# Kernel optimization log

Measured on AMD Instinct MI355X. Metric: run time of the kernel, lower is better.

Reference implementation:

```python
import jax, jax.numpy as jnp
import numpy as np

B, S, H = 32, 2048, 1024

def setup_inputs() -> dict:
    key = jax.random.key(0)
    k0, k1, k2, k3 = jax.random.split(key, 4)
    hidden = jax.random.normal(k0, (B, H), dtype=jnp.float32)
    encoder_outputs = jax.random.normal(k1, (S, B, H), dtype=jnp.float32)
    # torch nn.Linear weight layout: [out_features, in_features]
    attn_W = jax.random.normal(k2, (H, 2 * H), dtype=jnp.float32) * (1.0 / np.sqrt(2 * H))
    attn_b = jnp.zeros((H,), dtype=jnp.float32)
    v_W = jax.random.normal(k3, (1, H), dtype=jnp.float32) * (1.0 / np.sqrt(H))
    return {"hidden": hidden, "encoder_outputs": encoder_outputs,
            "attn_W": attn_W, "attn_b": attn_b, "v_W": v_W}

def reference(hidden, encoder_outputs, attn_W, attn_b, v_W):
    # encoder_outputs: [S, B, H] -> [B, S, H]
    enc = jnp.transpose(encoder_outputs, (1, 0, 2))
    b, s, h = enc.shape
    # broadcast decoder hidden across seq dim (avoids explicit repeat copy)
    hid = jnp.broadcast_to(hidden[:, None, :], (b, s, h))
    cat = jnp.concatenate([hid, enc], axis=2)              # [B, S, 2H]
    energy = jnp.tanh(jnp.einsum('bsk,hk->bsh', cat, attn_W) + attn_b)  # [B, S, H]
    scores = jnp.einsum('bsh,oh->bso', energy, v_W)[..., 0]            # [B, S]
    attn_weights = jax.nn.softmax(scores, axis=1)                       # [B, S]
    context = jnp.einsum('bs,bsh->bh', attn_weights, enc)               # [B, H]
    return context, attn_weights
```

## Files before the change

kernel.cpp:

```cpp
#include <hip/hip_runtime.h>
#include <hip/hip_bf16.h>
#include <cstddef>

#define B_ 32
#define S_ 2048
#define H_ 1024

typedef short short8 __attribute__((ext_vector_type(8)));
typedef float floatx4 __attribute__((ext_vector_type(4)));

__device__ inline unsigned int cvt_pk_bf16(float a, float b) {
    unsigned int r;
    asm("v_cvt_pk_bf16_f32 %0, %1, %2" : "=v"(r) : "v"(a), "v"(b));
    return r;
}

__device__ inline void gload_lds16(const unsigned short* g, unsigned short* l) {
    __builtin_amdgcn_global_load_lds(
        (const __attribute__((address_space(1))) unsigned int*)g,
        (__attribute__((address_space(3))) unsigned int*)l, 16, 0, 0);
}

__global__ void prep_kernel(const float* __restrict__ enc, unsigned short* __restrict__ encT,
                            const float* __restrict__ W, unsigned short* __restrict__ Bp) {
    int bid = blockIdx.x, t = threadIdx.x;
    if (bid < 32768) {
        int gtid = bid * 256 + t;
        int m = gtid >> 7, j7 = gtid & 127;
        const float4* p = reinterpret_cast<const float4*>(enc + (size_t)m * H_ + j7 * 8);
        float4 v0 = p[0], v1 = p[1];
        union { short8 s; unsigned int u[4]; } o;
        o.u[0] = cvt_pk_bf16(v0.x, v0.y);
        o.u[1] = cvt_pk_bf16(v0.z, v0.w);
        o.u[2] = cvt_pk_bf16(v1.x, v1.y);
        o.u[3] = cvt_pk_bf16(v1.z, v1.w);
        int tile = (m >> 7) * 16 + (j7 >> 3);
        int r = m & 127;
        int j = (j7 & 7) ^ (r & 7);
        reinterpret_cast<short8*>(encT)[(size_t)tile * 1024 + r * 8 + j] = o.s;
    } else {
        int gtid = (bid - 32768) * 256 + t;
        int n = gtid >> 7, j7 = gtid & 127;
        const float4* p = reinterpret_cast<const float4*>(W + (size_t)n * 2048 + 1024 + j7 * 8);
        float4 v0 = p[0], v1 = p[1];
        union { short8 s; unsigned int u[4]; } o;
        o.u[0] = cvt_pk_bf16(v0.x, v0.y);
        o.u[1] = cvt_pk_bf16(v0.z, v0.w);
        o.u[2] = cvt_pk_bf16(v1.x, v1.y);
        o.u[3] = cvt_pk_bf16(v1.z, v1.w);
        int nb = n >> 4, lr = n & 15, kt2 = j7 >> 2, lg = j7 & 3;
        reinterpret_cast<short8*>(Bp)[(nb * 32 + kt2) * 64 + lg * 16 + lr] = o.s;
    }
}

__global__ void hid_proj_kernel(const float* __restrict__ hidden,
                                const float* __restrict__ W,
                                const float* __restrict__ bias,
                                float* __restrict__ hp) {
    int h = blockIdx.x;
    int t = threadIdx.x;
    __shared__ float red[32][257];
    __shared__ float red2[32][8];
    float psum[32];
#pragma unroll
    for (int b = 0; b < 32; b++) psum[b] = 0.f;
    const float* wrow = W + (size_t)h * 2048;
    for (int c = 0; c < 4; c++) {
        int k = c * 256 + t;
        float w = wrow[k];
#pragma unroll
        for (int b = 0; b < 32; b++) psum[b] += hidden[b * 1024 + k] * w;
    }
#pragma unroll
    for (int b = 0; b < 32; b++) red[b][t] = psum[b];
    __syncthreads();
    {
        int b = t >> 3, j = t & 7;
        float s = 0.f;
#pragma unroll
        for (int q = 0; q < 32; q++) s += red[b][j * 32 + q];
        red2[b][j] = s;
    }
    __syncthreads();
    if (t < 32) {
        float tot = 0.f;
#pragma unroll
        for (int j = 0; j < 8; j++) tot += red2[t][j];
        hp[t * 1024 + h] = tot + bias[h];
    }
}

__global__ __launch_bounds__(256, 3) void score_gemm_t(
    const unsigned short* __restrict__ encT,
    const unsigned short* __restrict__ Bp,
    const float* __restrict__ hp,
    const float* __restrict__ vw,
    float* __restrict__ scores)
{
    __shared__ alignas(16) unsigned short As[2][8192];

    const int tid = threadIdx.x;
    const int lane = tid & 63;
    const int w = tid >> 6, wr = w >> 1, wc = w & 1;
    const int lr = lane & 15, lg = lane >> 4;
    const int lx = lr & 7;

    const int bid = blockIdx.x;
    const int x = bid & 7, j = bid >> 3;
    const int nt = j & 7;
    const int mt = (j >> 3) * 8 + x;

    const unsigned short* aT = encT + (size_t)mt * 16 * 8192;
    const short8* bp8 = reinterpret_cast<const short8*>(Bp);

    short8 bpf[2][8];
    {
        const unsigned short* src = aT + (w * 4) * 512 + lane * 8;
        unsigned short* dst = &As[0][(w * 4) * 512];
#pragma unroll
        for (int i = 0; i < 4; i++) gload_lds16(src + i * 512, dst + i * 512);
#pragma unroll
        for (int kk = 0; kk < 2; kk++)
#pragma unroll
            for (int ni = 0; ni < 4; ni++) {
                int nb = nt * 8 + wc * 4 + ni;
                bpf[0][kk * 4 + ni] = bp8[(nb * 32 + kk) * 64 + lane];
            }
    }

    floatx4 acc[4][4];
#pragma unroll
    for (int mi = 0; mi < 4; mi++)
#pragma unroll
        for (int ni = 0; ni < 4; ni++) acc[mi][ni] = (floatx4)0.f;

#pragma unroll
    for (int kt = 0; kt < 16; kt++) {
        const int cb = kt & 1;
        __syncthreads();
        if (kt < 15) {
            const unsigned short* src = aT + (kt + 1) * 8192 + (w * 4) * 512 + lane * 8;
            unsigned short* dst = &As[cb ^ 1][(w * 4) * 512];
#pragma unroll
            for (int i = 0; i < 4; i++) gload_lds16(src + i * 512, dst + i * 512);
#pragma unroll
            for (int kk = 0; kk < 2; kk++)
#pragma unroll
                for (int ni = 0; ni < 4; ni++) {
                    int nb = nt * 8 + wc * 4 + ni;
                    bpf[cb ^ 1][kk * 4 + ni] = bp8[(nb * 32 + (kt + 1) * 2 + kk) * 64 + lane];
                }
        }
#pragma unroll
        for (int kk = 0; kk < 2; kk++) {
            short8 afr[4];
#pragma unroll
            for (int mi = 0; mi < 4; mi++)
                afr[mi] = *reinterpret_cast<const short8*>(
                    &As[cb][(wr * 64 + mi * 16 + lr) * 64 + ((kk * 4 + lg) ^ lx) * 8]);
#pragma unroll
            for (int mi = 0; mi < 4; mi++)
#pragma unroll
                for (int ni = 0; ni < 4; ni++)
                    acc[mi][ni] = __builtin_amdgcn_mfma_f32_16x16x32_bf16(
                        afr[mi], bpf[cb][kk * 4 + ni], acc[mi][ni], 0, 0, 0);
        }
    }

    const int colBase = nt * 128 + wc * 64;
    float vv[4];
#pragma unroll
    for (int ni = 0; ni < 4; ni++) vv[ni] = vw[colBase + ni * 16 + lr];
#pragma unroll
    for (int mi = 0; mi < 4; mi++) {
        const int rowm = wr * 64 + mi * 16 + lg * 4;
#pragma unroll
        for (int i = 0; i < 4; i++) {
            const int m = mt * 128 + rowm + i;
            const int b = m & 31, sidx = m >> 5;
            const float* hprow = hp + b * H_ + colBase;
            float s = 0.f;
#pragma unroll
            for (int ni = 0; ni < 4; ni++) {
                float e = acc[mi][ni][i] + hprow[ni * 16 + lr];
                float e2 = __expf(2.0f * e);
                float th = 1.0f - 2.0f * __builtin_amdgcn_rcpf(e2 + 1.0f);
                s += th * vv[ni];
            }
            s += __shfl_xor(s, 1, 16);
            s += __shfl_xor(s, 2, 16);
            s += __shfl_xor(s, 4, 16);
            s += __shfl_xor(s, 8, 16);
            if (lr == 0) atomicAdd(&scores[b * S_ + sidx], s);
        }
    }
}

__global__ void softmax_kernel(const float* __restrict__ scores, float* __restrict__ out) {
    int b = blockIdx.x, t = threadIdx.x;
    __shared__ float red[16];
    const float* row = scores + b * S_;
    float vals[8];
    float lmax = -1e30f;
#pragma unroll
    for (int i = 0; i < 8; i++) { vals[i] = row[i * 256 + t]; lmax = fmaxf(lmax, vals[i]); }
#pragma unroll
    for (int off = 32; off; off >>= 1) lmax = fmaxf(lmax, __shfl_xor(lmax, off, 64));
    if ((t & 63) == 0) red[t >> 6] = lmax;
    __syncthreads();
    float gmax = fmaxf(fmaxf(red[0], red[1]), fmaxf(red[2], red[3]));
    float lsum = 0.f;
#pragma unroll
    for (int i = 0; i < 8; i++) { vals[i] = __expf(vals[i] - gmax); lsum += vals[i]; }
#pragma unroll
    for (int off = 32; off; off >>= 1) lsum += __shfl_xor(lsum, off, 64);
    if ((t & 63) == 0) red[8 + (t >> 6)] = lsum;
    __syncthreads();
    float inv = 1.0f / (red[8] + red[9] + red[10] + red[11]);
#pragma unroll
    for (int i = 0; i < 8; i++) out[b * S_ + i * 256 + t] = vals[i] * inv;
}

__global__ void context_tiled(const unsigned short* __restrict__ encT,
                              const float* __restrict__ wts,
                              float* __restrict__ ctx) {
    int t = threadIdx.x;
    int hc = blockIdx.x & 1;
    int b = (blockIdx.x >> 1) & 31;
    int sc = blockIdx.x >> 6;
    int h = hc * 512 + t * 2;
    const float* w = wts + b * S_ + sc * 128;
    const int jconst = ((h >> 3) & 7) ^ (b & 7);
    const int inrow = jconst * 8 + (h & 7);
    const int ktile = h >> 6;
    float acc0 = 0.f, acc1 = 0.f;
#pragma unroll 4
    for (int s = 0; s < 128; s++) {
        int m = (sc * 128 + s) * 32 + b;
        size_t off = ((size_t)(m >> 7) * 16 + ktile) * 8192 + (m & 127) * 64 + inrow;
        unsigned int u = *reinterpret_cast<const unsigned int*>(encT + off);
        float ws_ = w[s];
        acc0 += ws_ * __uint_as_float(u << 16);
        acc1 += ws_ * __uint_as_float(u & 0xffff0000u);
    }
    atomicAdd(&ctx[b * H_ + h], acc0);
    atomicAdd(&ctx[b * H_ + h + 1], acc1);
}

__global__ void pack_w2_rm(const float* __restrict__ W, unsigned short* __restrict__ W2) {
    int i = blockIdx.x * 256 + threadIdx.x;
    int n = i >> 8;
    int k4 = (i & 255) * 4;
    float4 v = *reinterpret_cast<const float4*>(W + (size_t)n * 2048 + 1024 + k4);
    uint2 o;
    o.x = cvt_pk_bf16(v.x, v.y);
    o.y = cvt_pk_bf16(v.z, v.w);
    *reinterpret_cast<uint2*>(W2 + (size_t)n * 1024 + k4) = o;
}

__global__ __launch_bounds__(256, 3) void score_gemm_f32(
    const float* __restrict__ Ap, const unsigned short* __restrict__ W2,
    const float* __restrict__ hp, const float* __restrict__ vw,
    float* __restrict__ scores)
{
    __shared__ alignas(16) unsigned short As[128 * 64];
    __shared__ alignas(16) unsigned short Bs[128 * 64];
    const int tid = threadIdx.x;
    const int lane = tid & 63;
    const int w = tid >> 6, wr = w >> 1, wc = w & 1;
    const int lr = lane & 15, lg = lane >> 4;
    const int bid = blockIdx.x;
    const int nt = bid & 7, mt = bid >> 3;
    const int row = tid >> 1, half = tid & 1;
    const int xk = row & 7;
    const int lx = lr & 7;
    const float* aF = Ap + (size_t)(mt * 128 + row) * H_ + half * 32;
    const unsigned short* bP = W2 + (size_t)(nt * 128 + row) * H_ + half * 32;
    short8 b8[4]; float4 af[8];
    {
        const float4* p = reinterpret_cast<const float4*>(aF);
#pragma unroll
        for (int i = 0; i < 8; i++) af[i] = p[i];
        const short8* q = reinterpret_cast<const short8*>(bP);
#pragma unroll
        for (int i = 0; i < 4; i++) b8[i] = q[i];
    }
    floatx4 acc[4][4];
#pragma unroll
    for (int mi = 0; mi < 4; mi++)
#pragma unroll
        for (int ni = 0; ni < 4; ni++) acc[mi][ni] = (floatx4)0.f;
    for (int kt = 0; kt < 16; kt++) {
        __syncthreads();
#pragma unroll
        for (int i = 0; i < 4; i++) {
            union { short8 s; unsigned int u[4]; } o;
            o.u[0] = cvt_pk_bf16(af[2 * i].x, af[2 * i].y);
            o.u[1] = cvt_pk_bf16(af[2 * i].z, af[2 * i].w);
            o.u[2] = cvt_pk_bf16(af[2 * i + 1].x, af[2 * i + 1].y);
            o.u[3] = cvt_pk_bf16(af[2 * i + 1].z, af[2 * i + 1].w);
            *reinterpret_cast<short8*>(&As[row * 64 + ((half * 4 + i) ^ xk) * 8]) = o.s;
        }
#pragma unroll
        for (int i = 0; i < 4; i++)
            *reinterpret_cast<short8*>(&Bs[row * 64 + ((half * 4 + i) ^ xk) * 8]) = b8[i];
        __syncthreads();
        if (kt < 15) {
            const float4* p = reinterpret_cast<const float4*>(aF + (kt + 1) * 64);
#pragma unroll
            for (int i = 0; i < 8; i++) af[i] = p[i];
            const short8* q = reinterpret_cast<const short8*>(bP + (kt + 1) * 64);
#pragma unroll
            for (int i = 0; i < 4; i++) b8[i] = q[i];
        }
#pragma unroll
        for (int kk = 0; kk < 2; kk++) {
            const int g = (kk * 4 + lg) ^ lx;
            short8 afr[4], bfr[4];
#pragma unroll
            for (int mi = 0; mi < 4; mi++)
                afr[mi] = *reinterpret_cast<const short8*>(&As[(wr * 64 + mi * 16 + lr) * 64 + g * 8]);
#pragma unroll
            for (int ni = 0; ni < 4; ni++)
                bfr[ni] = *reinterpret_cast<const short8*>(&Bs[(wc * 64 + ni * 16 + lr) * 64 + g * 8]);
#pragma unroll
            for (int mi = 0; mi < 4; mi++)
#pragma unroll
                for (int ni = 0; ni < 4; ni++)
                    acc[mi][ni] = __builtin_amdgcn_mfma_f32_16x16x32_bf16(
                        afr[mi], bfr[ni], acc[mi][ni], 0, 0, 0);
        }
    }
    const int colBase = nt * 128 + wc * 64;
    float vv[4];
#pragma unroll
    for (int ni = 0; ni < 4; ni++) vv[ni] = vw[colBase + ni * 16 + lr];
#pragma unroll
    for (int mi = 0; mi < 4; mi++) {
        const int rowm = wr * 64 + mi * 16 + lg * 4;
#pragma unroll
        for (int i = 0; i < 4; i++) {
            const int m = mt * 128 + rowm + i;
            const int b = m & 31, sidx = m >> 5;
            const float* hprow = hp + b * H_ + colBase;
            float s = 0.f;
#pragma unroll
            for (int ni = 0; ni < 4; ni++) {
                float e = acc[mi][ni][i] + hprow[ni * 16 + lr];
                float e2 = __expf(2.0f * e);
                float th = 1.0f - 2.0f * __builtin_amdgcn_rcpf(e2 + 1.0f);
                s += th * vv[ni];
            }
            s += __shfl_xor(s, 1, 16);
            s += __shfl_xor(s, 2, 16);
            s += __shfl_xor(s, 4, 16);
            s += __shfl_xor(s, 8, 16);
            if (lr == 0) atomicAdd(&scores[b * S_ + sidx], s);
        }
    }
}

__global__ void context_f32(const float* __restrict__ enc,
                            const float* __restrict__ wts,
                            float* __restrict__ ctx) {
    int t = threadIdx.x;
    int hc = blockIdx.x & 1;
    int b = (blockIdx.x >> 1) & 31;
    int sc = blockIdx.x >> 6;
    int h = hc * 512 + t * 2;
    const float* w = wts + b * S_ + sc * 128;
    const float* e = enc + (size_t)(sc * 128) * (B_ * H_) + b * H_ + h;
    float acc0 = 0.f, acc1 = 0.f;
#pragma unroll 8
    for (int s = 0; s < 128; s++) {
        float ws_ = w[s];
        acc0 += ws_ * e[(size_t)s * (B_ * H_)];
        acc1 += ws_ * e[(size_t)s * (B_ * H_) + 1];
    }
    atomicAdd(&ctx[b * H_ + h], acc0);
    atomicAdd(&ctx[b * H_ + h + 1], acc1);
}

extern "C" void kernel_launch(void* const* d_in, const int* in_sizes, int n_in,
                              void* d_out, int out_size, void* d_ws, size_t ws_size,
                              hipStream_t stream) {
    const float* hidden = (const float*)d_in[0];
    const float* enc    = (const float*)d_in[1];
    const float* attn_W = (const float*)d_in[2];
    const float* attn_b = (const float*)d_in[3];
    const float* v_W    = (const float*)d_in[4];
    float* out = (float*)d_out;

    char* ws = (char*)d_ws;
    const size_t ENCT_BYTES = (size_t)S_ * B_ * H_ * 2;
    const size_t BP_BYTES   = (size_t)H_ * H_ * 2;
    const bool big = ws_size >= ENCT_BYTES + BP_BYTES + (1u << 20);

    if (big) {
        unsigned short* encT = (unsigned short*)ws;
        unsigned short* Bp   = (unsigned short*)(ws + ENCT_BYTES);
        float* hp     = (float*)(ws + ENCT_BYTES + BP_BYTES);
        float* scores = (float*)(ws + ENCT_BYTES + BP_BYTES + (256u << 10));

        prep_kernel<<<33280, 256, 0, stream>>>(enc, encT, attn_W, Bp);
        hid_proj_kernel<<<1024, 256, 0, stream>>>(hidden, attn_W, attn_b, hp);
        hipMemsetAsync(scores, 0, B_ * S_ * sizeof(float), stream);
        score_gemm_t<<<4096, 256, 0, stream>>>(encT, Bp, hp, v_W, scores);
        softmax_kernel<<<32, 256, 0, stream>>>(scores, out + B_ * H_);
        hipMemsetAsync(out, 0, B_ * H_ * sizeof(float), stream);
        context_tiled<<<1024, 256, 0, stream>>>(encT, out + B_ * H_, out);
    } else {
        unsigned short* W2bf = (unsigned short*)ws;
        float* hp     = (float*)(ws + BP_BYTES);
        float* scores = (float*)(ws + BP_BYTES + (256u << 10));

        pack_w2_rm<<<1024, 256, 0, stream>>>(attn_W, W2bf);
        hid_proj_kernel<<<1024, 256, 0, stream>>>(hidden, attn_W, attn_b, hp);
        hipMemsetAsync(scores, 0, B_ * S_ * sizeof(float), stream);
        score_gemm_f32<<<4096, 256, 0, stream>>>(enc, W2bf, hp, v_W, scores);
        softmax_kernel<<<32, 256, 0, stream>>>(scores, out + B_ * H_);
        hipMemsetAsync(out, 0, B_ * H_ * sizeof(float), stream);
        context_f32<<<1024, 256, 0, stream>>>(enc, out + B_ * H_, out);
    }
}
```

Baseline: 635.4 us.

## Enlarge score GEMM tiles to 256x256 with 8 waves and phased MFMA pipeline

Replaces the 128x128-tile, 4-wave score GEMM with a 256x256-tile, 8-wave kernel. Each K tile is split into four phases that interleave global-to-LDS and B-fragment prefetch with MFMA bursts, using explicit barriers, waitcnt and setprio. Larger tiles halve how often A and B are re-read from global memory and cut the block count to 1024. In exchange it uses more registers and LDS per block, gives fewer blocks per CU, and relies on hand-placed waitcnt values being correct.

```diff
diff --git a/kernel.cpp b/kernel.cpp
--- a/kernel.cpp
+++ b/kernel.cpp
@@ -90,93 +90,138 @@
     }
 }
 
-__global__ __launch_bounds__(256, 3) void score_gemm_t(
+#define PHASE(CB, MI0, KK, STAGECODE, POSTCODE)                                    \
+  {                                                                                \
+    const unsigned short* ap_ =                                                    \
+        &As[CB][wr * 8192 + lr * 64 + ((((KK) * 4) + lg) ^ lx) * 8 + (MI0) * 1024];\
+    short8 afr_[4];                                                                \
+    _Pragma("unroll") for (int q_ = 0; q_ < 4; ++q_)                               \
+        afr_[q_] = *reinterpret_cast<const short8*>(ap_ + q_ * 1024);              \
+    STAGECODE                                                                      \
+    asm volatile("" ::: "memory");                                                 \
+    __builtin_amdgcn_s_barrier();                                                  \
+    asm volatile("s_waitcnt lgkmcnt(0)" ::: "memory");                             \
+    __builtin_amdgcn_sched_barrier(0);                                             \
+    __builtin_amdgcn_s_setprio(1);                                                 \
+    _Pragma("unroll") for (int q_ = 0; q_ < 4; ++q_) {                             \
+      _Pragma("unroll") for (int n_ = 0; n_ < 4; ++n_)                             \
+        acc[(MI0) + q_][n_] = __builtin_amdgcn_mfma_f32_16x16x32_bf16(             \
+            afr_[q_], bpf[CB][(KK) * 4 + n_], acc[(MI0) + q_][n_], 0, 0, 0);       \
+    }                                                                              \
+    __builtin_amdgcn_s_setprio(0);                                                 \
+    POSTCODE                                                                       \
+    __builtin_amdgcn_s_barrier();                                                  \
+  }
+
+#define KTILE(T, CB, ST)                                                           \
+  {                                                                                \
+    PHASE(CB, 0, 0,                                                                \
+      if (ST) {                                                                    \
+        const unsigned short* s_ = aSrc0 + (size_t)((T) + 1) * 8192;               \
+        unsigned short* d_ = (CB) ? dA00 : dA10;                                   \
+        gload_lds16(s_, d_);                                                       \
+        gload_lds16(s_ + 512, d_ + 512);                                           \
+      }, )                                                                         \
+    PHASE(CB, 4, 0,                                                                \
+      if (ST) {                                                                    \
+        const unsigned short* s_ = aSrc1 + (size_t)((T) + 1) * 8192;               \
+        unsigned short* d_ = (CB) ? dA01 : dA11;                                   \
+        gload_lds16(s_, d_);                                                       \
+        gload_lds16(s_ + 512, d_ + 512);                                           \
+        asm volatile("" ::: "memory");                                             \
+        const short8* bt_ = bpL + ((T) + 1) * 128;                                 \
+        bpf[(CB) ^ 1][0] = bt_[0];                                                 \
+        bpf[(CB) ^ 1][1] = bt_[2048];                                              \
+        bpf[(CB) ^ 1][2] = bt_[4096];                                              \
+        bpf[(CB) ^ 1][3] = bt_[6144];                                              \
+        bpf[(CB) ^ 1][4] = bt_[64];                                                \
+        bpf[(CB) ^ 1][5] = bt_[2112];                                              \
+        bpf[(CB) ^ 1][6] = bt_[4160];                                              \
+        bpf[(CB) ^ 1][7] = bt_[6208];                                              \
+      }, )                                                                         \
+    PHASE(CB, 0, 1, , )                                                            \
+    PHASE(CB, 4, 1, ,                                                              \
+      if (ST) { asm volatile("s_waitcnt vmcnt(8)" ::: "memory"); })                \
+  }
+
+__global__ __launch_bounds__(512, 2) void score_gemm_256(
     const unsigned short* __restrict__ encT,
     const unsigned short* __restrict__ Bp,
     const float* __restrict__ hp,
     const float* __restrict__ vw,
     float* __restrict__ scores)
 {
-    __shared__ alignas(16) unsigned short As[2][8192];
+    __shared__ alignas(16) unsigned short As[2][16384];
 
     const int tid = threadIdx.x;
     const int lane = tid & 63;
-    const int w = tid >> 6, wr = w >> 1, wc = w & 1;
+    const int w = tid >> 6;
+    const int wr = w >> 2, wc = w & 3;
     const int lr = lane & 15, lg = lane >> 4;
     const int lx = lr & 7;
 
     const int bid = blockIdx.x;
     const int x = bid & 7, j = bid >> 3;
-    const int nt = j & 7;
-    const int mt = (j >> 3) * 8 + x;
-
-    const unsigned short* aT = encT + (size_t)mt * 16 * 8192;
+    const int ntB = j & 3;
+    const int mtB = (j >> 2) * 8 + x;
+
+    const int segOff = w * 1024 + lane * 8;
+    const unsigned short* aSrc0 = encT + (size_t)(2 * mtB) * 131072 + segOff;
+    const unsigned short* aSrc1 = encT + (size_t)(2 * mtB + 1) * 131072 + segOff;
+    unsigned short* dA00 = &As[0][segOff];
+    unsigned short* dA01 = &As[0][8192 + segOff];
+    unsigned short* dA10 = &As[1][segOff];
+    unsigned short* dA11 = &As[1][8192 + segOff];
+
     const short8* bp8 = reinterpret_cast<const short8*>(Bp);
+    const int nbBase = ntB * 16 + wc * 4;
+    const short8* bpL = bp8 + (size_t)nbBase * 2048 + lane;
 
     short8 bpf[2][8];
+    floatx4 acc[8][4];
+#pragma unroll
+    for (int mi = 0; mi < 8; mi++)
+#pragma unroll
+        for (int ni = 0; ni < 4; ni++) acc[mi][ni] = (floatx4)0.f;
+
     {
-        const unsigned short* src = aT + (w * 4) * 512 + lane * 8;
-        unsigned short* dst = &As[0][(w * 4) * 512];
-#pragma unroll
-        for (int i = 0; i < 4; i++) gload_lds16(src + i * 512, dst + i * 512);
-#pragma unroll
-        for (int kk = 0; kk < 2; kk++)
-#pragma unroll
-            for (int ni = 0; ni < 4; ni++) {
-                int nb = nt * 8 + wc * 4 + ni;
-                bpf[0][kk * 4 + ni] = bp8[(nb * 32 + kk) * 64 + lane];
-            }
-    }
-
-    floatx4 acc[4][4];
-#pragma unroll
-    for (int mi = 0; mi < 4; mi++)
-#pragma unroll
-        for (int ni = 0; ni < 4; ni++) acc[mi][ni] = (floatx4)0.f;
-
-#pragma unroll
-    for (int kt = 0; kt < 16; kt++) {
-        const int cb = kt & 1;
-        __syncthreads();
-        if (kt < 15) {
-            const unsigned short* src = aT + (kt + 1) * 8192 + (w * 4) * 512 + lane * 8;
-            unsigned short* dst = &As[cb ^ 1][(w * 4) * 512];
-#pragma unroll
-            for (int i = 0; i < 4; i++) gload_lds16(src + i * 512, dst + i * 512);
-#pragma unroll
-            for (int kk = 0; kk < 2; kk++)
-#pragma unroll
-                for (int ni = 0; ni < 4; ni++) {
-                    int nb = nt * 8 + wc * 4 + ni;
-                    bpf[cb ^ 1][kk * 4 + ni] = bp8[(nb * 32 + (kt + 1) * 2 + kk) * 64 + lane];
-                }
-        }
-#pragma unroll
-        for (int kk = 0; kk < 2; kk++) {
-            short8 afr[4];
-#pragma unroll
-            for (int mi = 0; mi < 4; mi++)
-                afr[mi] = *reinterpret_cast<const short8*>(
-                    &As[cb][(wr * 64 + mi * 16 + lr) * 64 + ((kk * 4 + lg) ^ lx) * 8]);
-#pragma unroll
-            for (int mi = 0; mi < 4; mi++)
-#pragma unroll
-                for (int ni = 0; ni < 4; ni++)
-                    acc[mi][ni] = __builtin_amdgcn_mfma_f32_16x16x32_bf16(
-                        afr[mi], bpf[cb][kk * 4 + ni], acc[mi][ni], 0, 0, 0);
-        }
-    }
-
-    const int colBase = nt * 128 + wc * 64;
+        gload_lds16(aSrc0, dA00);
+        gload_lds16(aSrc0 + 512, dA00 + 512);
+        gload_lds16(aSrc1, dA01);
+        gload_lds16(aSrc1 + 512, dA01 + 512);
+        asm volatile("" ::: "memory");
+        bpf[0][0] = bpL[0];
+        bpf[0][1] = bpL[2048];
+        bpf[0][2] = bpL[4096];
+        bpf[0][3] = bpL[6144];
+        bpf[0][4] = bpL[64];
+        bpf[0][5] = bpL[2112];
+        bpf[0][6] = bpL[4160];
+        bpf[0][7] = bpL[6208];
+        asm volatile("" ::: "memory");
+        asm volatile("s_waitcnt vmcnt(8)" ::: "memory");
+        __builtin_amdgcn_s_barrier();
+    }
+
+#pragma unroll 1
+    for (int tt = 0; tt < 7; ++tt) {
+        const int t0 = tt * 2;
+        KTILE(t0, 0, true)
+        KTILE(t0 + 1, 1, true)
+    }
+    KTILE(14, 0, true)
+    KTILE(15, 1, false)
+
+    const int colBase = ntB * 256 + wc * 64;
     float vv[4];
 #pragma unroll
     for (int ni = 0; ni < 4; ni++) vv[ni] = vw[colBase + ni * 16 + lr];
 #pragma unroll
-    for (int mi = 0; mi < 4; mi++) {
-        const int rowm = wr * 64 + mi * 16 + lg * 4;
+    for (int mi = 0; mi < 8; mi++) {
+        const int rowm = wr * 128 + mi * 16 + lg * 4;
 #pragma unroll
         for (int i = 0; i < 4; i++) {
-            const int m = mt * 128 + rowm + i;
+            const int m = mtB * 256 + rowm + i;
             const int b = m & 31, sidx = m >> 5;
             const float* hprow = hp + b * H_ + colBase;
             float s = 0.f;
@@ -405,7 +450,7 @@
         prep_kernel<<<33280, 256, 0, stream>>>(enc, encT, attn_W, Bp);
         hid_proj_kernel<<<1024, 256, 0, stream>>>(hidden, attn_W, attn_b, hp);
         hipMemsetAsync(scores, 0, B_ * S_ * sizeof(float), stream);
-        score_gemm_t<<<4096, 256, 0, stream>>>(encT, Bp, hp, v_W, scores);
+        score_gemm_256<<<1024, 512, 0, stream>>>(encT, Bp, hp, v_W, scores);
         softmax_kernel<<<32, 256, 0, stream>>>(scores, out + B_ * H_);
         hipMemsetAsync(out, 0, B_ * H_ * sizeof(float), stream);
         context_tiled<<<1024, 256, 0, stream>>>(encT, out + B_ * H_, out);
```

Measured after the change: 707.9 us. +11.4%, slower.

## Fold output zeroing into prep kernel and retile context kernel with 16-byte loads

Applied to the files above, without the earlier changes.

The two hipMemsetAsync calls for scores and the context output are replaced by extra blocks in prep_kernel that write zeros, which removes two launches. The context kernel is rewritten so that each block covers a 64-wide H tile across all batches for 64 sequence positions. Attention weights are staged in LDS, and each thread reads 16-byte bf16 vectors and accumulates 8 outputs. This halves the block count and cuts per-element load overhead, at the cost of more atomics per thread and lower parallelism.

```diff
diff --git a/kernel.cpp b/kernel.cpp
--- a/kernel.cpp
+++ b/kernel.cpp
@@ -22,7 +22,8 @@
 }
 
 __global__ void prep_kernel(const float* __restrict__ enc, unsigned short* __restrict__ encT,
-                            const float* __restrict__ W, unsigned short* __restrict__ Bp) {
+                            const float* __restrict__ W, unsigned short* __restrict__ Bp,
+                            float* __restrict__ scores, float* __restrict__ ctx) {
     int bid = blockIdx.x, t = threadIdx.x;
     if (bid < 32768) {
         int gtid = bid * 256 + t;
@@ -38,7 +39,7 @@
         int r = m & 127;
         int j = (j7 & 7) ^ (r & 7);
         reinterpret_cast<short8*>(encT)[(size_t)tile * 1024 + r * 8 + j] = o.s;
-    } else {
+    } else if (bid < 33280) {
         int gtid = (bid - 32768) * 256 + t;
         int n = gtid >> 7, j7 = gtid & 127;
         const float4* p = reinterpret_cast<const float4*>(W + (size_t)n * 2048 + 1024 + j7 * 8);
@@ -50,6 +51,11 @@
         o.u[3] = cvt_pk_bf16(v1.z, v1.w);
         int nb = n >> 4, lr = n & 15, kt2 = j7 >> 2, lg = j7 & 3;
         reinterpret_cast<short8*>(Bp)[(nb * 32 + kt2) * 64 + lg * 16 + lr] = o.s;
+    } else {
+        int z = bid - 33280;
+        float4 zero = {0.f, 0.f, 0.f, 0.f};
+        if (z < 64) reinterpret_cast<float4*>(scores)[z * 256 + t] = zero;
+        else        reinterpret_cast<float4*>(ctx)[(z - 64) * 256 + t] = zero;
     }
 }
 
@@ -221,30 +227,48 @@
     for (int i = 0; i < 8; i++) out[b * S_ + i * 256 + t] = vals[i] * inv;
 }
 
-__global__ void context_tiled(const unsigned short* __restrict__ encT,
-                              const float* __restrict__ wts,
-                              float* __restrict__ ctx) {
-    int t = threadIdx.x;
-    int hc = blockIdx.x & 1;
-    int b = (blockIdx.x >> 1) & 31;
-    int sc = blockIdx.x >> 6;
-    int h = hc * 512 + t * 2;
-    const float* w = wts + b * S_ + sc * 128;
-    const int jconst = ((h >> 3) & 7) ^ (b & 7);
-    const int inrow = jconst * 8 + (h & 7);
-    const int ktile = h >> 6;
-    float acc0 = 0.f, acc1 = 0.f;
+__global__ void context_tiled2(const unsigned short* __restrict__ encT,
+                               const float* __restrict__ wts,
+                               float* __restrict__ ctx) {
+    __shared__ float wsh[32][65];
+    const int t = threadIdx.x;
+    const int kt = blockIdx.x & 15;
+    const int s0 = (blockIdx.x >> 4) * 64;
+    const int b = t >> 3, c = t & 7;
+    const int cx = c ^ (b & 7);
+
+#pragma unroll
+    for (int i = 0; i < 8; i++) {
+        int idx = i * 256 + t;
+        wsh[idx >> 6][idx & 63] = wts[(idx >> 6) * S_ + s0 + (idx & 63)];
+    }
+    __syncthreads();
+
+    float acc[8];
+#pragma unroll
+    for (int e = 0; e < 8; e++) acc[e] = 0.f;
+
+    const size_t tileBase = ((size_t)(s0 >> 2) * 16 + kt) * 8192;
 #pragma unroll 4
-    for (int s = 0; s < 128; s++) {
-        int m = (sc * 128 + s) * 32 + b;
-        size_t off = ((size_t)(m >> 7) * 16 + ktile) * 8192 + (m & 127) * 64 + inrow;
-        unsigned int u = *reinterpret_cast<const unsigned int*>(encT + off);
-        float ws_ = w[s];
-        acc0 += ws_ * __uint_as_float(u << 16);
-        acc1 += ws_ * __uint_as_float(u & 0xffff0000u);
-    }
-    atomicAdd(&ctx[b * H_ + h], acc0);
-    atomicAdd(&ctx[b * H_ + h + 1], acc1);
+    for (int i = 0; i < 64; i++) {
+        size_t off = tileBase + (size_t)(i >> 2) * 131072
+                   + ((i & 3) * 32 + b) * 64 + cx * 8;
+        union { short8 s8; unsigned int u[4]; } v;
+        v.s8 = *reinterpret_cast<const short8*>(encT + off);
+        float w = wsh[b][i];
+        acc[0] += w * __uint_as_float(v.u[0] << 16);
+        acc[1] += w * __uint_as_float(v.u[0] & 0xffff0000u);
+        acc[2] += w * __uint_as_float(v.u[1] << 16);
+        acc[3] += w * __uint_as_float(v.u[1] & 0xffff0000u);
+        acc[4] += w * __uint_as_float(v.u[2] << 16);
+        acc[5] += w * __uint_as_float(v.u[2] & 0xffff0000u);
+        acc[6] += w * __uint_as_float(v.u[3] << 16);
+        acc[7] += w * __uint_as_float(v.u[3] & 0xffff0000u);
+    }
+
+    const int hbase = kt * 64 + c * 8;
+#pragma unroll
+    for (int e = 0; e < 8; e++) atomicAdd(&ctx[b * H_ + hbase + e], acc[e]);
 }
 
 __global__ void pack_w2_rm(const float* __restrict__ W, unsigned short* __restrict__ W2) {
@@ -402,13 +426,11 @@
         float* hp     = (float*)(ws + ENCT_BYTES + BP_BYTES);
         float* scores = (float*)(ws + ENCT_BYTES + BP_BYTES + (256u << 10));
 
-        prep_kernel<<<33280, 256, 0, stream>>>(enc, encT, attn_W, Bp);
+        prep_kernel<<<33376, 256, 0, stream>>>(enc, encT, attn_W, Bp, scores, out);
         hid_proj_kernel<<<1024, 256, 0, stream>>>(hidden, attn_W, attn_b, hp);
-        hipMemsetAsync(scores, 0, B_ * S_ * sizeof(float), stream);
         score_gemm_t<<<4096, 256, 0, stream>>>(encT, Bp, hp, v_W, scores);
         softmax_kernel<<<32, 256, 0, stream>>>(scores, out + B_ * H_);
-        hipMemsetAsync(out, 0, B_ * H_ * sizeof(float), stream);
-        context_tiled<<<1024, 256, 0, stream>>>(encT, out + B_ * H_, out);
+        context_tiled2<<<512, 256, 0, stream>>>(encT, out + B_ * H_, out);
     } else {
         unsigned short* W2bf = (unsigned short*)ws;
         float* hp     = (float*)(ws + BP_BYTES);
```

Result: slower. 663.6 us (+4.5%).

## Deepen GEMM prefetch pipeline and fold memsets into prep kernel

Applied to the files above, without the earlier changes.

The score GEMM now prefetches two K-tiles ahead, with explicit vmcnt waits and split barriers instead of one __syncthreads per iteration, so global-to-LDS loads overlap more with the MFMA work. MFMA blocks are wrapped in s_setprio to favour the math waves. The two hipMemsetAsync calls are removed and the zeroing of the scores and context buffers is folded into extra blocks of the prep kernel, which cuts launch overhead. The hand-written waitcnt counts are fragile and depend on how the compiler orders the loads.

```diff
diff --git a/kernel.cpp b/kernel.cpp
--- a/kernel.cpp
+++ b/kernel.cpp
@@ -22,7 +22,8 @@
 }
 
 __global__ void prep_kernel(const float* __restrict__ enc, unsigned short* __restrict__ encT,
-                            const float* __restrict__ W, unsigned short* __restrict__ Bp) {
+                            const float* __restrict__ W, unsigned short* __restrict__ Bp,
+                            float* __restrict__ scores, float* __restrict__ ctx) {
     int bid = blockIdx.x, t = threadIdx.x;
     if (bid < 32768) {
         int gtid = bid * 256 + t;
@@ -38,7 +39,7 @@
         int r = m & 127;
         int j = (j7 & 7) ^ (r & 7);
         reinterpret_cast<short8*>(encT)[(size_t)tile * 1024 + r * 8 + j] = o.s;
-    } else {
+    } else if (bid < 33280) {
         int gtid = (bid - 32768) * 256 + t;
         int n = gtid >> 7, j7 = gtid & 127;
         const float4* p = reinterpret_cast<const float4*>(W + (size_t)n * 2048 + 1024 + j7 * 8);
@@ -50,6 +51,11 @@
         o.u[3] = cvt_pk_bf16(v1.z, v1.w);
         int nb = n >> 4, lr = n & 15, kt2 = j7 >> 2, lg = j7 & 3;
         reinterpret_cast<short8*>(Bp)[(nb * 32 + kt2) * 64 + lg * 16 + lr] = o.s;
+    } else {
+        int z = bid - 33280;
+        float4 zero = {0.f, 0.f, 0.f, 0.f};
+        if (z < 64) reinterpret_cast<float4*>(scores)[z * 256 + t] = zero;
+        else        reinterpret_cast<float4*>(ctx)[(z - 64) * 256 + t] = zero;
     }
 }
 
@@ -112,45 +118,41 @@
 
     const unsigned short* aT = encT + (size_t)mt * 16 * 8192;
     const short8* bp8 = reinterpret_cast<const short8*>(Bp);
+    const unsigned short* aSrc = aT + (w * 4) * 512 + lane * 8;
+    unsigned short* aDst0 = &As[0][(w * 4) * 512];
+    unsigned short* aDst1 = &As[1][(w * 4) * 512];
+    const int nbB = nt * 8 + wc * 4;
 
     short8 bpf[2][8];
+    floatx4 acc[4][4];
+#pragma unroll
+    for (int mi = 0; mi < 4; mi++)
+#pragma unroll
+        for (int ni = 0; ni < 4; ni++) acc[mi][ni] = (floatx4)0.f;
+
     {
-        const unsigned short* src = aT + (w * 4) * 512 + lane * 8;
-        unsigned short* dst = &As[0][(w * 4) * 512];
-#pragma unroll
-        for (int i = 0; i < 4; i++) gload_lds16(src + i * 512, dst + i * 512);
+#pragma unroll
+        for (int i = 0; i < 4; i++) gload_lds16(aSrc + i * 512, aDst0 + i * 512);
 #pragma unroll
         for (int kk = 0; kk < 2; kk++)
 #pragma unroll
-            for (int ni = 0; ni < 4; ni++) {
-                int nb = nt * 8 + wc * 4 + ni;
-                bpf[0][kk * 4 + ni] = bp8[(nb * 32 + kk) * 64 + lane];
-            }
-    }
-
-    floatx4 acc[4][4];
-#pragma unroll
-    for (int mi = 0; mi < 4; mi++)
-#pragma unroll
-        for (int ni = 0; ni < 4; ni++) acc[mi][ni] = (floatx4)0.f;
+            for (int ni = 0; ni < 4; ni++)
+                bpf[0][kk * 4 + ni] = bp8[((nbB + ni) * 32 + kk) * 64 + lane];
+#pragma unroll
+        for (int i = 0; i < 4; i++) gload_lds16(aSrc + 8192 + i * 512, aDst1 + i * 512);
+#pragma unroll
+        for (int kk = 0; kk < 2; kk++)
+#pragma unroll
+            for (int ni = 0; ni < 4; ni++)
+                bpf[1][kk * 4 + ni] = bp8[((nbB + ni) * 32 + 2 + kk) * 64 + lane];
+        asm volatile("s_waitcnt vmcnt(12)" ::: "memory");
+        __builtin_amdgcn_s_barrier();
+        asm volatile("" ::: "memory");
+    }
 
 #pragma unroll
     for (int kt = 0; kt < 16; kt++) {
         const int cb = kt & 1;
-        __syncthreads();
-        if (kt < 15) {
-            const unsigned short* src = aT + (kt + 1) * 8192 + (w * 4) * 512 + lane * 8;
-            unsigned short* dst = &As[cb ^ 1][(w * 4) * 512];
-#pragma unroll
-            for (int i = 0; i < 4; i++) gload_lds16(src + i * 512, dst + i * 512);
-#pragma unroll
-            for (int kk = 0; kk < 2; kk++)
-#pragma unroll
-                for (int ni = 0; ni < 4; ni++) {
-                    int nb = nt * 8 + wc * 4 + ni;
-                    bpf[cb ^ 1][kk * 4 + ni] = bp8[(nb * 32 + (kt + 1) * 2 + kk) * 64 + lane];
-                }
-        }
 #pragma unroll
         for (int kk = 0; kk < 2; kk++) {
             short8 afr[4];
@@ -158,12 +160,37 @@
             for (int mi = 0; mi < 4; mi++)
                 afr[mi] = *reinterpret_cast<const short8*>(
                     &As[cb][(wr * 64 + mi * 16 + lr) * 64 + ((kk * 4 + lg) ^ lx) * 8]);
+            __builtin_amdgcn_s_setprio(1);
 #pragma unroll
             for (int mi = 0; mi < 4; mi++)
 #pragma unroll
                 for (int ni = 0; ni < 4; ni++)
                     acc[mi][ni] = __builtin_amdgcn_mfma_f32_16x16x32_bf16(
                         afr[mi], bpf[cb][kk * 4 + ni], acc[mi][ni], 0, 0, 0);
+            __builtin_amdgcn_s_setprio(0);
+        }
+        if (kt < 14) {
+            __builtin_amdgcn_s_barrier();
+            asm volatile("" ::: "memory");
+            {
+                const unsigned short* src = aSrc + (kt + 2) * 8192;
+                unsigned short* dst = cb ? aDst1 : aDst0;
+#pragma unroll
+                for (int i = 0; i < 4; i++) gload_lds16(src + i * 512, dst + i * 512);
+#pragma unroll
+                for (int kk = 0; kk < 2; kk++)
+#pragma unroll
+                    for (int ni = 0; ni < 4; ni++)
+                        bpf[cb][kk * 4 + ni] =
+                            bp8[((nbB + ni) * 32 + (kt + 2) * 2 + kk) * 64 + lane];
+            }
+            asm volatile("s_waitcnt vmcnt(12)" ::: "memory");
+            __builtin_amdgcn_s_barrier();
+            asm volatile("" ::: "memory");
+        } else if (kt == 14) {
+            asm volatile("s_waitcnt vmcnt(0)" ::: "memory");
+            __builtin_amdgcn_s_barrier();
+            asm volatile("" ::: "memory");
         }
     }
 
@@ -402,12 +429,10 @@
         float* hp     = (float*)(ws + ENCT_BYTES + BP_BYTES);
         float* scores = (float*)(ws + ENCT_BYTES + BP_BYTES + (256u << 10));
 
-        prep_kernel<<<33280, 256, 0, stream>>>(enc, encT, attn_W, Bp);
+        prep_kernel<<<33376, 256, 0, stream>>>(enc, encT, attn_W, Bp, scores, out);
         hid_proj_kernel<<<1024, 256, 0, stream>>>(hidden, attn_W, attn_b, hp);
-        hipMemsetAsync(scores, 0, B_ * S_ * sizeof(float), stream);
         score_gemm_t<<<4096, 256, 0, stream>>>(encT, Bp, hp, v_W, scores);
         softmax_kernel<<<32, 256, 0, stream>>>(scores, out + B_ * H_);
-        hipMemsetAsync(out, 0, B_ * H_ * sizeof(float), stream);
         context_tiled<<<1024, 256, 0, stream>>>(encT, out + B_ * H_, out);
     } else {
         unsigned short* W2bf = (unsigned short*)ws;
```

Result: slower. 658.7 us (+3.7%).
